# Optimization experiments

Measured on AMD Instinct MI355X. Metric: run time of the kernel, lower is better.

## Reference

```python
import jax, jax.numpy as jnp
import numpy as np

N_NODES = 50000

def setup_inputs() -> dict:
    key = jax.random.key(0)
    ks = jax.random.split(key, 8)
    d_in, d_h = 128, 128
    x = jax.random.normal(ks[0], (N_NODES, d_in), dtype=jnp.float32)
    edge_index = jax.random.randint(ks[1], (2, 800000), 0, N_NODES, dtype=jnp.int64)
    edge_pairs = jax.random.randint(ks[2], (1000000, 2), 0, N_NODES, dtype=jnp.int64)
    W_gcn = jax.random.normal(ks[3], (d_in, d_h), dtype=jnp.float32) / np.sqrt(d_in)
    b_gcn = jnp.zeros((d_h,), dtype=jnp.float32)
    W1 = jax.random.normal(ks[4], (2 * d_h, d_h), dtype=jnp.float32) / np.sqrt(2 * d_h)
    b1 = jnp.zeros((d_h,), dtype=jnp.float32)
    W2 = jax.random.normal(ks[5], (d_h, 1), dtype=jnp.float32) / np.sqrt(d_h)
    b2 = jnp.zeros((1,), dtype=jnp.float32)
    return {"x": x, "edge_index": edge_index, "edge_pairs": edge_pairs,
            "W_gcn": W_gcn, "b_gcn": b_gcn, "W1": W1, "b1": b1, "W2": W2, "b2": b2}

def gcn_conv(x, edge_index, W, b):
    # PyG GCNConv default: add self-loops, symmetric normalization.
    n = x.shape[0]
    loop = jnp.arange(n, dtype=edge_index.dtype)
    src = jnp.concatenate([edge_index[0], loop])  # [E+N]
    dst = jnp.concatenate([edge_index[1], loop])
    deg = jax.ops.segment_sum(jnp.ones(src.shape[0], dtype=x.dtype), dst, num_segments=n)
    dinv = jnp.where(deg > 0, jax.lax.rsqrt(deg), 0.0)
    norm = dinv[src] * dinv[dst]                  # [E+N]
    h = x @ W                                     # [N, H]
    agg = jax.ops.segment_sum(h[src] * norm[:, None], dst, num_segments=n)
    return agg + b

def reference(x, edge_index, edge_pairs, W_gcn, b_gcn, W1, b1, W2, b2):
    h = gcn_conv(x, edge_index, W_gcn, b_gcn)      # [N, H]
    e = jnp.concatenate([h[edge_pairs[:, 0]], h[edge_pairs[:, 1]]], axis=-1)  # [P, 2H]
    edge_logits = jax.nn.relu(e @ W1 + b1) @ W2 + b2  # [P, 1]
    return edge_logits, edge_pairs, h
```

## Files before the change

kernel.cpp:

```cpp
#include <hip/hip_runtime.h>
#include <hip/hip_fp16.h>

#define WG 256

typedef _Float16 f16;
typedef _Float16 hv2 __attribute__((ext_vector_type(2)));
typedef _Float16 f16x4 __attribute__((ext_vector_type(4)));
typedef _Float16 f16x8 __attribute__((ext_vector_type(8)));
typedef float f32x4 __attribute__((ext_vector_type(4)));

__global__ __launch_bounds__(WG) void k_deg_init(int* __restrict__ deg, int n) {
    int i = blockIdx.x * WG + threadIdx.x;
    if (i < n) deg[i] = 1;
}

__global__ __launch_bounds__(WG) void k_deg_count(const int* __restrict__ dst,
                                                  int* __restrict__ deg, int e) {
    int i = blockIdx.x * WG + threadIdx.x;
    if (i < e) atomicAdd(&deg[dst[i]], 1);
}

__global__ __launch_bounds__(WG) void k_scan1(const int* __restrict__ deg,
                                              float* __restrict__ dinv,
                                              int* __restrict__ base,
                                              int* __restrict__ bsum, int n) {
    __shared__ int t[WG];
    int tid = threadIdx.x;
    int i = blockIdx.x * WG + tid;
    int d = (i < n) ? deg[i] : 1;
    if (i < n) dinv[i] = rsqrtf((float)d);
    int v = (i < n) ? d - 1 : 0;
    t[tid] = v;
    __syncthreads();
    for (int o = 1; o < WG; o <<= 1) {
        int add = (tid >= o) ? t[tid - o] : 0;
        __syncthreads();
        t[tid] += add;
        __syncthreads();
    }
    if (i < n) base[i] = t[tid] - v;
    if (tid == WG - 1) bsum[blockIdx.x] = t[WG - 1];
}

__global__ __launch_bounds__(WG) void k_scan2(int* __restrict__ bsum, int nb) {
    __shared__ int t[WG];
    int tid = threadIdx.x;
    int v = (tid < nb) ? bsum[tid] : 0;
    t[tid] = v;
    __syncthreads();
    for (int o = 1; o < WG; o <<= 1) {
        int add = (tid >= o) ? t[tid - o] : 0;
        __syncthreads();
        t[tid] += add;
        __syncthreads();
    }
    if (tid < nb) bsum[tid] = t[tid] - v;
}

__global__ __launch_bounds__(WG) void k_scan3(int* __restrict__ base,
                                              const int* __restrict__ bsum,
                                              int* __restrict__ cursor, int n, int e) {
    int i = blockIdx.x * WG + threadIdx.x;
    if (i < n) {
        int b = base[i] + bsum[blockIdx.x];
        base[i] = b;
        cursor[i] = b;
        if (i == n - 1) base[n] = e;
    }
}

__global__ __launch_bounds__(WG) void k_fill(const int* __restrict__ src,
                                             const int* __restrict__ dst,
                                             const float* __restrict__ dinv,
                                             int* __restrict__ cursor,
                                             int* __restrict__ esrc,
                                             float* __restrict__ ew, int e) {
    int i = blockIdx.x * WG + threadIdx.x;
    if (i >= e) return;
    int s = src[i], d = dst[i];
    int pos = atomicAdd(&cursor[d], 1);
    esrc[pos] = s;
    ew[pos] = dinv[s] * dinv[d];
}

__global__ __launch_bounds__(WG) void k_transpose(const float* __restrict__ src,
                                                  f16* __restrict__ dst, int logk) {
    int i = blockIdx.x * WG + threadIdx.x;
    int K = 1 << logk;
    int k = i & (K - 1), nI = i >> logk;
    dst[i] = (f16)src[(size_t)k * 128 + nI];
}

__global__ __launch_bounds__(WG) void k_mm_hpk(const float* __restrict__ A,
                                               const f16* __restrict__ Wt,
                                               __half2* __restrict__ Out, int n) {
    __shared__ f16 As[64][136];
    __shared__ f16 Bs[128][136];
    const int tid = threadIdx.x;
    const int row0 = blockIdx.x * 64;
    for (int f = tid; f < 128 * 16; f += WG) {
        int r = f >> 4, c = f & 15;
        *(float4*)&Bs[r][c * 8] = ((const float4*)Wt)[r * 16 + c];
    }
    for (int f = tid; f < 64 * 32; f += WG) {
        int r = f >> 5, c = f & 31;
        float4 v = make_float4(0.f, 0.f, 0.f, 0.f);
        if (row0 + r < n) v = ((const float4*)A)[(size_t)(row0 + r) * 32 + c];
        *(f16x4*)&As[r][c * 4] = (f16x4){(f16)v.x, (f16)v.y, (f16)v.z, (f16)v.w};
    }
    __syncthreads();
    const int wv = tid >> 6, lane = tid & 63, m = lane & 15, quad = lane >> 4;
    f32x4 acc[8];
#pragma unroll
    for (int t = 0; t < 8; ++t) acc[t] = (f32x4){0.f, 0.f, 0.f, 0.f};
#pragma unroll
    for (int kk = 0; kk < 4; ++kk) {
        f16x8 af = *(f16x8*)&As[wv * 16 + m][kk * 32 + quad * 8];
#pragma unroll
        for (int t = 0; t < 8; ++t) {
            f16x8 bf = *(f16x8*)&Bs[t * 16 + m][kk * 32 + quad * 8];
            acc[t] = __builtin_amdgcn_mfma_f32_16x16x32_f16(af, bf, acc[t], 0, 0, 0);
        }
    }
#pragma unroll
    for (int t = 0; t < 4; ++t)
#pragma unroll
        for (int r = 0; r < 4; ++r) {
            int row = row0 + wv * 16 + quad * 4 + r;
            if (row < n)
                Out[(size_t)row * 64 + t * 16 + m] = __floats2half2_rn(acc[t][r], acc[t + 4][r]);
        }
}

__global__ __launch_bounds__(WG) void k_mm_uv(const float* __restrict__ A,
                                              const f16* __restrict__ W1t,
                                              const float* __restrict__ b1,
                                              __half2* __restrict__ Up,
                                              __half2* __restrict__ Vp, int n) {
    __shared__ f16 As[64][136];
    __shared__ f16 Bs[128][136];
    const int tid = threadIdx.x;
    const int row0 = blockIdx.x * 64;
    for (int f = tid; f < 64 * 32; f += WG) {
        int r = f >> 5, c = f & 31;
        float4 v = make_float4(0.f, 0.f, 0.f, 0.f);
        if (row0 + r < n) v = ((const float4*)A)[(size_t)(row0 + r) * 32 + c];
        *(f16x4*)&As[r][c * 4] = (f16x4){(f16)v.x, (f16)v.y, (f16)v.z, (f16)v.w};
    }
    const int wv = tid >> 6, lane = tid & 63, m = lane & 15, quad = lane >> 4;
    f32x4 acc[8];
#pragma unroll
    for (int ph = 0; ph < 2; ++ph) {
        if (ph) __syncthreads();
        for (int f = tid; f < 128 * 16; f += WG) {
            int r = f >> 4, c = f & 15;
            *(float4*)&Bs[r][c * 8] = *(const float4*)(W1t + (size_t)r * 256 + ph * 128 + c * 8);
        }
        __syncthreads();
#pragma unroll
        for (int t = 0; t < 8; ++t) acc[t] = (f32x4){0.f, 0.f, 0.f, 0.f};
#pragma unroll
        for (int kk = 0; kk < 4; ++kk) {
            f16x8 af = *(f16x8*)&As[wv * 16 + m][kk * 32 + quad * 8];
#pragma unroll
            for (int t = 0; t < 8; ++t) {
                f16x8 bf = *(f16x8*)&Bs[t * 16 + m][kk * 32 + quad * 8];
                acc[t] = __builtin_amdgcn_mfma_f32_16x16x32_f16(af, bf, acc[t], 0, 0, 0);
            }
        }
        __half2* Out = ph ? Vp : Up;
#pragma unroll
        for (int t = 0; t < 4; ++t) {
            float bl = 0.f, bh = 0.f;
            if (!ph) { bl = b1[t * 16 + m]; bh = b1[t * 16 + m + 64]; }
#pragma unroll
            for (int r = 0; r < 4; ++r) {
                int row = row0 + wv * 16 + quad * 4 + r;
                if (row < n)
                    Out[(size_t)row * 64 + t * 16 + m] =
                        __floats2half2_rn(acc[t][r] + bl, acc[t + 4][r] + bh);
            }
        }
    }
}

__global__ __launch_bounds__(WG) void k_gather(const __half2* __restrict__ Hpk,
                                               const float* __restrict__ dinv,
                                               const float* __restrict__ bg,
                                               const int* __restrict__ base,
                                               const int* __restrict__ esrc,
                                               const float* __restrict__ ew,
                                               float* __restrict__ outh, int n) {
    int tid = threadIdx.x;
    int node = blockIdx.x * 16 + (tid >> 4);
    int sub = tid & 15;
    if (node >= n) return;
    float dv = dinv[node];
    float s2 = dv * dv;
    float4 blo = *(const float4*)(bg + 4 * sub);
    float4 bhi = *(const float4*)(bg + 4 * sub + 64);
    int4 hh = *(const int4*)(Hpk + (size_t)node * 64 + 4 * sub);
    const int* hp = (const int*)&hh;
    float accl[4], acch[4];
#pragma unroll
    for (int k = 0; k < 4; ++k) {
        hv2 h = __builtin_bit_cast(hv2, hp[k]);
        accl[k] = fmaf((float)h[0], s2, ((const float*)&blo)[k]);
        acch[k] = fmaf((float)h[1], s2, ((const float*)&bhi)[k]);
    }
    int j = base[node], jend = base[node + 1];
    for (; j + 4 <= jend; j += 4) {
        int s0 = esrc[j], s1 = esrc[j + 1], s2i = esrc[j + 2], s3 = esrc[j + 3];
        float w0 = ew[j], w1 = ew[j + 1], w2 = ew[j + 2], w3 = ew[j + 3];
        int4 r0 = *(const int4*)(Hpk + (size_t)s0 * 64 + 4 * sub);
        int4 r1 = *(const int4*)(Hpk + (size_t)s1 * 64 + 4 * sub);
        int4 r2 = *(const int4*)(Hpk + (size_t)s2i * 64 + 4 * sub);
        int4 r3 = *(const int4*)(Hpk + (size_t)s3 * 64 + 4 * sub);
        const int* p0 = (const int*)&r0;
        const int* p1 = (const int*)&r1;
        const int* p2 = (const int*)&r2;
        const int* p3 = (const int*)&r3;
#pragma unroll
        for (int k = 0; k < 4; ++k) {
            hv2 h0 = __builtin_bit_cast(hv2, p0[k]);
            hv2 h1 = __builtin_bit_cast(hv2, p1[k]);
            hv2 h2 = __builtin_bit_cast(hv2, p2[k]);
            hv2 h3 = __builtin_bit_cast(hv2, p3[k]);
            accl[k] = fmaf((float)h0[0], w0, accl[k]); acch[k] = fmaf((float)h0[1], w0, acch[k]);
            accl[k] = fmaf((float)h1[0], w1, accl[k]); acch[k] = fmaf((float)h1[1], w1, acch[k]);
            accl[k] = fmaf((float)h2[0], w2, accl[k]); acch[k] = fmaf((float)h2[1], w2, acch[k]);
            accl[k] = fmaf((float)h3[0], w3, accl[k]); acch[k] = fmaf((float)h3[1], w3, acch[k]);
        }
    }
    for (; j < jend; ++j) {
        int s = esrc[j];
        float w = ew[j];
        int4 r = *(const int4*)(Hpk + (size_t)s * 64 + 4 * sub);
        const int* pr = (const int*)&r;
#pragma unroll
        for (int k = 0; k < 4; ++k) {
            hv2 h = __builtin_bit_cast(hv2, pr[k]);
            accl[k] = fmaf((float)h[0], w, accl[k]);
            acch[k] = fmaf((float)h[1], w, acch[k]);
        }
    }
    *(float4*)&outh[(size_t)node * 128 + 4 * sub] =
        make_float4(accl[0], accl[1], accl[2], accl[3]);
    *(float4*)&outh[(size_t)node * 128 + 64 + 4 * sub] =
        make_float4(acch[0], acch[1], acch[2], acch[3]);
}

__global__ __launch_bounds__(WG) void k_pair8(const __half2* __restrict__ U,
                                              const __half2* __restrict__ V,
                                              const float* __restrict__ W2,
                                              const float* __restrict__ b2,
                                              const int* __restrict__ pairs,
                                              float* __restrict__ out_logit, int p) {
    int wv = (blockIdx.x * WG + threadIdx.x) >> 6;
    int lane = threadIdx.x & 63;
    int g = lane >> 4, sub = lane & 15;
    int q0 = wv * 8 + g, q1 = q0 + 4;
    bool v0 = (q0 < p), v1 = (q1 < p);
    if (!v0) return;
    int qa0 = q0, qa1 = v1 ? q1 : q0;
    int a0 = pairs[2 * qa0], b0 = pairs[2 * qa0 + 1];
    int a1 = pairs[2 * qa1], b1i = pairs[2 * qa1 + 1];

    float4 w2lo = ((const float4*)W2)[sub];
    float4 w2hi = ((const float4*)(W2 + 64))[sub];
    hv2 w2h[4];
    w2h[0] = hv2{(f16)w2lo.x, (f16)w2hi.x};
    w2h[1] = hv2{(f16)w2lo.y, (f16)w2hi.y};
    w2h[2] = hv2{(f16)w2lo.z, (f16)w2hi.z};
    w2h[3] = hv2{(f16)w2lo.w, (f16)w2hi.w};

    int4 u0 = *(const int4*)(U + (size_t)a0 * 64 + 4 * sub);
    int4 vv0 = *(const int4*)(V + (size_t)b0 * 64 + 4 * sub);
    int4 u1 = *(const int4*)(U + (size_t)a1 * 64 + 4 * sub);
    int4 vv1 = *(const int4*)(V + (size_t)b1i * 64 + 4 * sub);
    const int* ui0 = (const int*)&u0;
    const int* vi0 = (const int*)&vv0;
    const int* ui1 = (const int*)&u1;
    const int* vi1 = (const int*)&vv1;

    const hv2 z2 = hv2{(f16)0.f, (f16)0.f};
    float p0 = 0.f, p1 = 0.f;
#pragma unroll
    for (int k = 0; k < 4; ++k) {
        hv2 s0 = __builtin_bit_cast(hv2, ui0[k]) + __builtin_bit_cast(hv2, vi0[k]);
        hv2 s1 = __builtin_bit_cast(hv2, ui1[k]) + __builtin_bit_cast(hv2, vi1[k]);
        p0 = __builtin_amdgcn_fdot2(__builtin_elementwise_max(s0, z2), w2h[k], p0, false);
        p1 = __builtin_amdgcn_fdot2(__builtin_elementwise_max(s1, z2), w2h[k], p1, false);
    }
#pragma unroll
    for (int m = 1; m < 16; m <<= 1) {
        p0 += __shfl_xor(p0, m, 64);
        p1 += __shfl_xor(p1, m, 64);
    }
    if (sub == 0) {
        float bb = b2[0];
        out_logit[q0] = p0 + bb;
        if (v1) out_logit[q1] = p1 + bb;
    }
}

__global__ __launch_bounds__(WG) void k_cvtpairs(const int* __restrict__ pairs,
                                                 float* __restrict__ outp, int n4) {
    int i = blockIdx.x * WG + threadIdx.x;
    if (i >= n4) return;
    int4 v = ((const int4*)pairs)[i];
    ((float4*)outp)[i] = make_float4((float)v.x, (float)v.y, (float)v.z, (float)v.w);
}

extern "C" void kernel_launch(void* const* d_in, const int* in_sizes, int n_in,
                              void* d_out, int out_size, void* d_ws, size_t ws_size,
                              hipStream_t stream) {
    const float* x     = (const float*)d_in[0];
    const int*   eidx  = (const int*)d_in[1];
    const int*   pairs = (const int*)d_in[2];
    const float* W_gcn = (const float*)d_in[3];
    const float* b_gcn = (const float*)d_in[4];
    const float* W1    = (const float*)d_in[5];
    const float* b1    = (const float*)d_in[6];
    const float* W2    = (const float*)d_in[7];
    const float* b2    = (const float*)d_in[8];

    const int N = in_sizes[0] / 128;
    const int E = in_sizes[1] / 2;
    const int P = in_sizes[2] / 2;
    const int* esrc_in = eidx;
    const int* edst_in = eidx + E;

    float* ws      = (float*)d_ws;
    int*   deg     = (int*)d_ws;
    float* dinv    = ws + 65536;
    int*   base    = (int*)(ws + 131072);
    int*   cursor  = (int*)(ws + 196608);
    int*   bsum    = (int*)(ws + 262144);
    f16*   Wt_gcn  = (f16*)(ws + 262400);
    f16*   W1t     = (f16*)(ws + 270592);
    int*   ecsr    = (int*)(ws + 287744);
    float* ew      = ws + 287744 + E;
    __half2* Hpk   = (__half2*)(ws + 287744 + 2 * (size_t)E);
    __half2* Upk   = Hpk + (size_t)N * 64;
    __half2* Vpk   = Upk + (size_t)N * 64;

    float* out_logit = (float*)d_out;
    float* out_pairs = out_logit + P;
    float* out_h     = out_logit + 3 * (size_t)P;

    const int nb = (N + WG - 1) / WG;
    dim3 blk(WG);
    dim3 grid_pair((unsigned)((P + 31) / 32));
    k_deg_init  <<<nb, blk, 0, stream>>>(deg, N);
    k_deg_count <<<(E + WG - 1) / WG, blk, 0, stream>>>(edst_in, deg, E);
    k_scan1     <<<nb, blk, 0, stream>>>(deg, dinv, base, bsum, N);
    k_scan2     <<<1,  blk, 0, stream>>>(bsum, nb);
    k_scan3     <<<nb, blk, 0, stream>>>(base, bsum, cursor, N, E);
    k_fill      <<<(E + WG - 1) / WG, blk, 0, stream>>>(esrc_in, edst_in, dinv, cursor, ecsr, ew, E);
    k_transpose <<<(128 * 128) / WG, blk, 0, stream>>>(W_gcn, Wt_gcn, 7);
    k_transpose <<<(128 * 256) / WG, blk, 0, stream>>>(W1, W1t, 8);
    k_mm_hpk    <<<(N + 63) / 64, blk, 0, stream>>>(x, Wt_gcn, Hpk, N);
    k_gather    <<<(N + 15) / 16, blk, 0, stream>>>(Hpk, dinv, b_gcn, base, ecsr, ew, out_h, N);
    k_mm_uv     <<<(N + 63) / 64, blk, 0, stream>>>(out_h, W1t, b1, Upk, Vpk, N);
    k_cvtpairs  <<<(P / 2 + WG - 1) / WG, blk, 0, stream>>>(pairs, out_pairs, P / 2);
    k_pair8     <<<grid_pair, blk, 0, stream>>>(Upk, Vpk, W2, b2, pairs, out_logit, P);
}
```

Baseline: 324.8 us.

## Fold GCN normalization into matmul epilogue and drop per-edge weights

The symmetric normalization dinv[s]*dinv[d] is factored: the source-side dinv is applied to H in the matmul epilogue and the destination-side dinv once per node after an unweighted neighbor sum. This removes the per-edge weight array, its writes in the fill kernel, and its reads in the gather loop, cutting memory traffic and FMA work. The degree-init kernel is replaced by a memset, with the self-loop counted as +1 in the scan. Storing the pre-scaled H in fp16 slightly changes rounding.

```diff
diff --git a/kernel.cpp b/kernel.cpp
--- a/kernel.cpp
+++ b/kernel.cpp
@@ -8,11 +8,6 @@
 typedef _Float16 f16x4 __attribute__((ext_vector_type(4)));
 typedef _Float16 f16x8 __attribute__((ext_vector_type(8)));
 typedef float f32x4 __attribute__((ext_vector_type(4)));
-
-__global__ __launch_bounds__(WG) void k_deg_init(int* __restrict__ deg, int n) {
-    int i = blockIdx.x * WG + threadIdx.x;
-    if (i < n) deg[i] = 1;
-}
 
 __global__ __launch_bounds__(WG) void k_deg_count(const int* __restrict__ dst,
                                                   int* __restrict__ deg, int e) {
@@ -27,9 +22,8 @@
     __shared__ int t[WG];
     int tid = threadIdx.x;
     int i = blockIdx.x * WG + tid;
-    int d = (i < n) ? deg[i] : 1;
-    if (i < n) dinv[i] = rsqrtf((float)d);
-    int v = (i < n) ? d - 1 : 0;
+    int v = (i < n) ? deg[i] : 0;
+    if (i < n) dinv[i] = rsqrtf((float)(v + 1));
     t[tid] = v;
     __syncthreads();
     for (int o = 1; o < WG; o <<= 1) {
@@ -71,16 +65,13 @@
 
 __global__ __launch_bounds__(WG) void k_fill(const int* __restrict__ src,
                                              const int* __restrict__ dst,
-                                             const float* __restrict__ dinv,
                                              int* __restrict__ cursor,
-                                             int* __restrict__ esrc,
-                                             float* __restrict__ ew, int e) {
+                                             int* __restrict__ esrc, int e) {
     int i = blockIdx.x * WG + threadIdx.x;
     if (i >= e) return;
     int s = src[i], d = dst[i];
     int pos = atomicAdd(&cursor[d], 1);
     esrc[pos] = s;
-    ew[pos] = dinv[s] * dinv[d];
 }
 
 __global__ __launch_bounds__(WG) void k_transpose(const float* __restrict__ src,
@@ -93,6 +84,7 @@
 
 __global__ __launch_bounds__(WG) void k_mm_hpk(const float* __restrict__ A,
                                                const f16* __restrict__ Wt,
+                                               const float* __restrict__ dinv,
                                                __half2* __restrict__ Out, int n) {
     __shared__ f16 As[64][136];
     __shared__ f16 Bs[128][136];
@@ -123,13 +115,16 @@
         }
     }
 #pragma unroll
-    for (int t = 0; t < 4; ++t)
-#pragma unroll
-        for (int r = 0; r < 4; ++r) {
-            int row = row0 + wv * 16 + quad * 4 + r;
-            if (row < n)
-                Out[(size_t)row * 64 + t * 16 + m] = __floats2half2_rn(acc[t][r], acc[t + 4][r]);
-        }
+    for (int r = 0; r < 4; ++r) {
+        int row = row0 + wv * 16 + quad * 4 + r;
+        if (row < n) {
+            float dv = dinv[row];
+#pragma unroll
+            for (int t = 0; t < 4; ++t)
+                Out[(size_t)row * 64 + t * 16 + m] =
+                    __floats2half2_rn(acc[t][r] * dv, acc[t + 4][r] * dv);
+        }
+    }
 }
 
 __global__ __launch_bounds__(WG) void k_mm_uv(const float* __restrict__ A,
@@ -189,29 +184,23 @@
                                                const float* __restrict__ bg,
                                                const int* __restrict__ base,
                                                const int* __restrict__ esrc,
-                                               const float* __restrict__ ew,
                                                float* __restrict__ outh, int n) {
     int tid = threadIdx.x;
     int node = blockIdx.x * 16 + (tid >> 4);
     int sub = tid & 15;
     if (node >= n) return;
-    float dv = dinv[node];
-    float s2 = dv * dv;
-    float4 blo = *(const float4*)(bg + 4 * sub);
-    float4 bhi = *(const float4*)(bg + 4 * sub + 64);
     int4 hh = *(const int4*)(Hpk + (size_t)node * 64 + 4 * sub);
     const int* hp = (const int*)&hh;
     float accl[4], acch[4];
 #pragma unroll
     for (int k = 0; k < 4; ++k) {
         hv2 h = __builtin_bit_cast(hv2, hp[k]);
-        accl[k] = fmaf((float)h[0], s2, ((const float*)&blo)[k]);
-        acch[k] = fmaf((float)h[1], s2, ((const float*)&bhi)[k]);
+        accl[k] = (float)h[0];
+        acch[k] = (float)h[1];
     }
     int j = base[node], jend = base[node + 1];
     for (; j + 4 <= jend; j += 4) {
         int s0 = esrc[j], s1 = esrc[j + 1], s2i = esrc[j + 2], s3 = esrc[j + 3];
-        float w0 = ew[j], w1 = ew[j + 1], w2 = ew[j + 2], w3 = ew[j + 3];
         int4 r0 = *(const int4*)(Hpk + (size_t)s0 * 64 + 4 * sub);
         int4 r1 = *(const int4*)(Hpk + (size_t)s1 * 64 + 4 * sub);
         int4 r2 = *(const int4*)(Hpk + (size_t)s2i * 64 + 4 * sub);
@@ -226,28 +215,30 @@
             hv2 h1 = __builtin_bit_cast(hv2, p1[k]);
             hv2 h2 = __builtin_bit_cast(hv2, p2[k]);
             hv2 h3 = __builtin_bit_cast(hv2, p3[k]);
-            accl[k] = fmaf((float)h0[0], w0, accl[k]); acch[k] = fmaf((float)h0[1], w0, acch[k]);
-            accl[k] = fmaf((float)h1[0], w1, accl[k]); acch[k] = fmaf((float)h1[1], w1, acch[k]);
-            accl[k] = fmaf((float)h2[0], w2, accl[k]); acch[k] = fmaf((float)h2[1], w2, acch[k]);
-            accl[k] = fmaf((float)h3[0], w3, accl[k]); acch[k] = fmaf((float)h3[1], w3, acch[k]);
+            accl[k] += (float)h0[0] + (float)h1[0] + (float)h2[0] + (float)h3[0];
+            acch[k] += (float)h0[1] + (float)h1[1] + (float)h2[1] + (float)h3[1];
         }
     }
     for (; j < jend; ++j) {
         int s = esrc[j];
-        float w = ew[j];
         int4 r = *(const int4*)(Hpk + (size_t)s * 64 + 4 * sub);
         const int* pr = (const int*)&r;
 #pragma unroll
         for (int k = 0; k < 4; ++k) {
             hv2 h = __builtin_bit_cast(hv2, pr[k]);
-            accl[k] = fmaf((float)h[0], w, accl[k]);
-            acch[k] = fmaf((float)h[1], w, acch[k]);
-        }
-    }
+            accl[k] += (float)h[0];
+            acch[k] += (float)h[1];
+        }
+    }
+    float dv = dinv[node];
+    float4 blo = *(const float4*)(bg + 4 * sub);
+    float4 bhi = *(const float4*)(bg + 4 * sub + 64);
     *(float4*)&outh[(size_t)node * 128 + 4 * sub] =
-        make_float4(accl[0], accl[1], accl[2], accl[3]);
+        make_float4(fmaf(accl[0], dv, blo.x), fmaf(accl[1], dv, blo.y),
+                    fmaf(accl[2], dv, blo.z), fmaf(accl[3], dv, blo.w));
     *(float4*)&outh[(size_t)node * 128 + 64 + 4 * sub] =
-        make_float4(acch[0], acch[1], acch[2], acch[3]);
+        make_float4(fmaf(acch[0], dv, bhi.x), fmaf(acch[1], dv, bhi.y),
+                    fmaf(acch[2], dv, bhi.z), fmaf(acch[3], dv, bhi.w));
 }
 
 __global__ __launch_bounds__(WG) void k_pair8(const __half2* __restrict__ U,
@@ -340,8 +331,7 @@
     f16*   Wt_gcn  = (f16*)(ws + 262400);
     f16*   W1t     = (f16*)(ws + 270592);
     int*   ecsr    = (int*)(ws + 287744);
-    float* ew      = ws + 287744 + E;
-    __half2* Hpk   = (__half2*)(ws + 287744 + 2 * (size_t)E);
+    __half2* Hpk   = (__half2*)(ws + 287744 + (size_t)E);
     __half2* Upk   = Hpk + (size_t)N * 64;
     __half2* Vpk   = Upk + (size_t)N * 64;
 
@@ -352,16 +342,16 @@
     const int nb = (N + WG - 1) / WG;
     dim3 blk(WG);
     dim3 grid_pair((unsigned)((P + 31) / 32));
-    k_deg_init  <<<nb, blk, 0, stream>>>(deg, N);
+    hipMemsetAsync(deg, 0, (size_t)N * 4, stream);
     k_deg_count <<<(E + WG - 1) / WG, blk, 0, stream>>>(edst_in, deg, E);
     k_scan1     <<<nb, blk, 0, stream>>>(deg, dinv, base, bsum, N);
     k_scan2     <<<1,  blk, 0, stream>>>(bsum, nb);
     k_scan3     <<<nb, blk, 0, stream>>>(base, bsum, cursor, N, E);
-    k_fill      <<<(E + WG - 1) / WG, blk, 0, stream>>>(esrc_in, edst_in, dinv, cursor, ecsr, ew, E);
+    k_fill      <<<(E + WG - 1) / WG, blk, 0, stream>>>(esrc_in, edst_in, cursor, ecsr, E);
     k_transpose <<<(128 * 128) / WG, blk, 0, stream>>>(W_gcn, Wt_gcn, 7);
     k_transpose <<<(128 * 256) / WG, blk, 0, stream>>>(W1, W1t, 8);
-    k_mm_hpk    <<<(N + 63) / 64, blk, 0, stream>>>(x, Wt_gcn, Hpk, N);
-    k_gather    <<<(N + 15) / 16, blk, 0, stream>>>(Hpk, dinv, b_gcn, base, ecsr, ew, out_h, N);
+    k_mm_hpk    <<<(N + 63) / 64, blk, 0, stream>>>(x, Wt_gcn, dinv, Hpk, N);
+    k_gather    <<<(N + 15) / 16, blk, 0, stream>>>(Hpk, dinv, b_gcn, base, ecsr, out_h, N);
     k_mm_uv     <<<(N + 63) / 64, blk, 0, stream>>>(out_h, W1t, b1, Upk, Vpk, N);
     k_cvtpairs  <<<(P / 2 + WG - 1) / WG, blk, 0, stream>>>(pairs, out_pairs, P / 2);
     k_pair8     <<<grid_pair, blk, 0, stream>>>(Upk, Vpk, W2, b2, pairs, out_logit, P);
```

Measured after the change: 316.3 us. -2.6%, faster.
